# Optimization experiments

Measured on AMD Instinct MI355X. Metric: run time of the kernel, lower is better.

Reference implementation:

```python
import jax, jax.numpy as jnp
import numpy as np

EPS = 1e-6
TOP_K = 2


def setup_inputs() -> dict:
    key = jax.random.key(0)
    k0, k1, k2, k3, k4 = jax.random.split(key, 5)
    B, S, H, I, E = 1, 2048, 1024, 3584, 8
    return {
        "hidden_states": jax.random.normal(k0, (B, S, H), jnp.float32),
        "rms_weight": jnp.ones((H,), jnp.float32),
        "gate_w": jax.random.normal(k1, (E, H), jnp.float32) * (H ** -0.5),
        "w1": jax.random.normal(k2, (E, I, H), jnp.float32) * (H ** -0.5),
        "w2": jax.random.normal(k3, (E, H, I), jnp.float32) * (I ** -0.5),
        "w3": jax.random.normal(k4, (E, I, H), jnp.float32) * (H ** -0.5),
    }


def reference(hidden_states, rms_weight, gate_w, w1, w2, w3):
    B, S, H = hidden_states.shape
    E = gate_w.shape[0]
    # RMSNorm (fp32 internally, matches _RMSNorm)
    x = hidden_states.astype(jnp.float32)
    var = jnp.mean(x * x, axis=-1, keepdims=True)
    h = rms_weight * (x * jax.lax.rsqrt(var + EPS))  # [B,S,H]
    # Router: softmax over experts, top-k, renormalize
    logits = jnp.einsum('bsh,eh->bse', h, gate_w)
    scores = jax.nn.softmax(logits.astype(jnp.float32), axis=-1)
    top_w, top_i = jax.lax.top_k(scores, TOP_K)        # [B,S,K]
    top_w = top_w / jnp.sum(top_w, axis=-1, keepdims=True)
    top_w = top_w.astype(h.dtype)
    # Per-token combine weight for every expert: cw[t,e]
    hf = h.reshape(-1, H)                               # [T,H]
    oh = jax.nn.one_hot(top_i.reshape(-1, TOP_K), E, dtype=h.dtype)  # [T,K,E]
    cw = jnp.einsum('tke,tk->te', oh, top_w.reshape(-1, TOP_K))       # [T,E]
    # SwiGLU expert MLPs, batched over experts (dense dispatch; weights zero out unrouted tokens)
    a = jnp.einsum('th,eih->eti', hf, w1)               # [E,T,I]
    g = jnp.einsum('th,eih->eti', hf, w3)               # [E,T,I]
    eo = jnp.einsum('eti,ehi->eth', jax.nn.silu(a) * g, w2)  # [E,T,H]
    out = jnp.einsum('eth,te->th', eo, cw)              # [T,H]
    return hidden_states + out.reshape(B, S, H)
```

## Files before the change

### kernel.cpp

```cpp
#include <hip/hip_runtime.h>
#include <hip/hip_bf16.h>
#include <stdint.h>

#define T_TOK 2048
#define HDIM  1024
#define IDIM  3584
#define NEXP  8
#define NROWS 4096

typedef __attribute__((ext_vector_type(8))) short bf16x8;
typedef __attribute__((ext_vector_type(4))) float f32x4;
typedef __attribute__((ext_vector_type(4))) unsigned int u32x4;

__device__ __forceinline__ unsigned short f2bf(float f){
  union { float f; unsigned u; } v; v.f = f;
  unsigned r = v.u + 0x7FFFu + ((v.u >> 16) & 1u);
  return (unsigned short)(r >> 16);
}

__device__ __forceinline__ u32x4 pack8(float4 lo, float4 hi){
  union { unsigned short s[8]; u32x4 v; } u;
  u.s[0]=f2bf(lo.x); u.s[1]=f2bf(lo.y); u.s[2]=f2bf(lo.z); u.s[3]=f2bf(lo.w);
  u.s[4]=f2bf(hi.x); u.s[5]=f2bf(hi.y); u.s[6]=f2bf(hi.z); u.s[7]=f2bf(hi.w);
  return u.v;
}

__global__ __launch_bounds__(256) void k_rms_router(
    const float* __restrict__ x, const float* __restrict__ rmsw,
    const float* __restrict__ gw, unsigned short* __restrict__ h_bf,
    int* __restrict__ topk_i, float* __restrict__ topk_w, int* __restrict__ count)
{
  const int t = blockIdx.x, tid = threadIdx.x;
  const int lane = tid & 63, wid = tid >> 6;
  float4 x4 = reinterpret_cast<const float4*>(x)[t*256 + tid];
  float ss = x4.x*x4.x + x4.y*x4.y + x4.z*x4.z + x4.w*x4.w;
  #pragma unroll
  for (int o = 32; o >= 1; o >>= 1) ss += __shfl_xor(ss, o);
  __shared__ float sred[4];
  __shared__ float slog[32];
  if (lane == 0) sred[wid] = ss;
  __syncthreads();
  float inv = rsqrtf((sred[0]+sred[1]+sred[2]+sred[3]) * (1.0f/HDIM) + 1e-6f);
  float4 w4 = reinterpret_cast<const float4*>(rmsw)[tid];
  float h0 = x4.x*inv*w4.x, h1 = x4.y*inv*w4.y, h2 = x4.z*inv*w4.z, h3 = x4.w*inv*w4.w;
  ushort4 hb; hb.x = f2bf(h0); hb.y = f2bf(h1); hb.z = f2bf(h2); hb.w = f2bf(h3);
  reinterpret_cast<ushort4*>(h_bf)[t*256 + tid] = hb;
  #pragma unroll
  for (int e = 0; e < NEXP; e++){
    float4 g4 = reinterpret_cast<const float4*>(gw)[e*256 + tid];
    float v = h0*g4.x + h1*g4.y + h2*g4.z + h3*g4.w;
    #pragma unroll
    for (int o = 32; o >= 1; o >>= 1) v += __shfl_xor(v, o);
    if (lane == 0) slog[e*4 + wid] = v;
  }
  __syncthreads();
  if (tid == 0){
    float lg[NEXP];
    #pragma unroll
    for (int e = 0; e < NEXP; e++) lg[e] = slog[e*4]+slog[e*4+1]+slog[e*4+2]+slog[e*4+3];
    int i0 = 0;
    for (int e = 1; e < NEXP; e++) if (lg[e] > lg[i0]) i0 = e;
    int i1 = -1;
    for (int e = 0; e < NEXP; e++){ if (e == i0) continue; if (i1 < 0 || lg[e] > lg[i1]) i1 = e; }
    float m  = fmaxf(lg[i0], lg[i1]);
    float e0 = expf(lg[i0]-m), e1 = expf(lg[i1]-m);
    float s  = e0 + e1;
    topk_i[t*2] = i0; topk_i[t*2+1] = i1;
    topk_w[t*2] = e0/s; topk_w[t*2+1] = e1/s;
    atomicAdd(&count[i0], 1); atomicAdd(&count[i1], 1);
  }
}

__global__ void k_scan(const int* __restrict__ count, int* __restrict__ offset){
  if (threadIdx.x == 0){
    int o = 0;
    for (int e = 0; e < NEXP; e++){ offset[e] = o; o += count[e]; }
  }
}

__global__ __launch_bounds__(256) void k_scatter(
    const int* __restrict__ topk_i, const float* __restrict__ topk_w,
    const int* __restrict__ offset, int* __restrict__ cursor,
    int* __restrict__ token_of_row, float* __restrict__ wrow, int* __restrict__ slot_of)
{
  int t = blockIdx.x*256 + threadIdx.x;
  if (t >= T_TOK) return;
  #pragma unroll
  for (int k = 0; k < 2; k++){
    int e = topk_i[t*2+k];
    int pos = atomicAdd(&cursor[e], 1);
    int row = offset[e] + pos;
    token_of_row[row] = t;
    wrow[row] = topk_w[t*2+k];
    slot_of[t*2+k] = row;
  }
}

__global__ __launch_bounds__(256, 3) void k_mlp_in(
    const unsigned short* __restrict__ h_bf, const float* __restrict__ w1,
    const float* __restrict__ w3, const int* __restrict__ token_of_row,
    const int* __restrict__ count, const int* __restrict__ offset,
    unsigned short* __restrict__ act)
{
  int bx, by, bz;
  {
    int d = blockIdx.x + 16*(blockIdx.y + 56*blockIdx.z);
    int w = (d & 7)*896 + (d >> 3);
    bx = w & 15; int r = w >> 4; by = r % 56; bz = r / 56;
  }
  const int e = bz;
  const int tile = bx;
  const int cnt = count[e];
  if (tile * 128 >= cnt) return;
  const int off  = offset[e];
  const int row0 = off + tile*128;
  const int rend = off + cnt;
  const int col0 = by * 64;
  const int tid = threadIdx.x, lane = tid & 63, wid = tid >> 6;
  const int wave_r = wid >> 1, wave_c = wid & 1;

  __shared__ __align__(16) char sA [128*128];
  __shared__ __align__(16) char sB1[64*128];
  __shared__ __align__(16) char sB2[64*128];

  const int arow_base = tid >> 3;
  const int kseg = tid & 7;
  const unsigned short* aptr[4];
  #pragma unroll
  for (int j = 0; j < 4; j++){
    int r = row0 + arow_base + 32*j;
    aptr[j] = h_bf + (size_t)token_of_row[min(r, NROWS-1)]*HDIM + kseg*8;
  }
  const float* w1base = w1 + (size_t)e*IDIM*HDIM + (size_t)col0*HDIM + (size_t)arow_base*HDIM + kseg*8;
  const float* w3base = w3 + (size_t)e*IDIM*HDIM + (size_t)col0*HDIM + (size_t)arow_base*HDIM + kseg*8;

  u32x4  pa[4];
  float4 pb1[2][2], pb3[2][2];

  auto LOAD = [&](int kk){
    #pragma unroll
    for (int j = 0; j < 4; j++)
      pa[j] = *reinterpret_cast<const u32x4*>(aptr[j] + kk*64);
    #pragma unroll
    for (int j = 0; j < 2; j++){
      const float4* p1 = reinterpret_cast<const float4*>(w1base + (size_t)(32*j)*HDIM + kk*64);
      const float4* p3 = reinterpret_cast<const float4*>(w3base + (size_t)(32*j)*HDIM + kk*64);
      pb1[j][0] = p1[0]; pb1[j][1] = p1[1];
      pb3[j][0] = p3[0]; pb3[j][1] = p3[1];
    }
  };
  const int aswz = (kseg ^ (arow_base & 7)) << 4;
  auto STORE = [&](){
    #pragma unroll
    for (int j = 0; j < 4; j++)
      *reinterpret_cast<u32x4*>(sA + (arow_base + 32*j)*128 + aswz) = pa[j];
    #pragma unroll
    for (int j = 0; j < 2; j++){
      *reinterpret_cast<u32x4*>(sB1 + (arow_base + 32*j)*128 + aswz) = pack8(pb1[j][0], pb1[j][1]);
      *reinterpret_cast<u32x4*>(sB2 + (arow_base + 32*j)*128 + aswz) = pack8(pb3[j][0], pb3[j][1]);
    }
  };

  f32x4 acc_a[4][2], acc_g[4][2];
  #pragma unroll
  for (int m = 0; m < 4; m++)
    #pragma unroll
    for (int n = 0; n < 2; n++){
      acc_a[m][n] = (f32x4){0.f,0.f,0.f,0.f};
      acc_g[m][n] = (f32x4){0.f,0.f,0.f,0.f};
    }

  LOAD(0);
  for (int kk = 0; kk < HDIM/64; kk++){
    STORE();
    if (kk + 1 < HDIM/64) LOAD(kk+1);
    __syncthreads();
    #pragma unroll
    for (int ki = 0; ki < 2; ki++){
      bf16x8 af[4];
      #pragma unroll
      for (int m = 0; m < 4; m++){
        int row = wave_r*64 + m*16 + (lane&15);
        int slot = ki*4 + (lane>>4);
        af[m] = *reinterpret_cast<const bf16x8*>(sA + row*128 + ((slot ^ (row&7))<<4));
      }
      #pragma unroll
      for (int n = 0; n < 2; n++){
        int col = wave_c*32 + n*16 + (lane&15);
        int slot = ki*4 + (lane>>4);
        bf16x8 b1 = *reinterpret_cast<const bf16x8*>(sB1 + col*128 + ((slot ^ (col&7))<<4));
        bf16x8 b2 = *reinterpret_cast<const bf16x8*>(sB2 + col*128 + ((slot ^ (col&7))<<4));
        #pragma unroll
        for (int m = 0; m < 4; m++){
          acc_a[m][n] = __builtin_amdgcn_mfma_f32_16x16x32_bf16(af[m], b1, acc_a[m][n], 0,0,0);
          acc_g[m][n] = __builtin_amdgcn_mfma_f32_16x16x32_bf16(af[m], b2, acc_g[m][n], 0,0,0);
        }
      }
    }
    __syncthreads();
  }
  const int lcol = lane & 15, lrow4 = (lane >> 4) * 4;
  #pragma unroll
  for (int m = 0; m < 4; m++){
    #pragma unroll
    for (int n = 0; n < 2; n++){
      int gcol = col0 + wave_c*32 + n*16 + lcol;
      #pragma unroll
      for (int r = 0; r < 4; r++){
        int grow = row0 + wave_r*64 + m*16 + lrow4 + r;
        if (grow < rend){
          float a = acc_a[m][n][r], g = acc_g[m][n][r];
          float sig = 1.0f / (1.0f + __expf(-a));
          act[(size_t)grow*IDIM + gcol] = f2bf(a * sig * g);
        }
      }
    }
  }
}

__global__ __launch_bounds__(256, 4) void k_mlp_out(
    const unsigned short* __restrict__ act, const float* __restrict__ w2,
    const float* __restrict__ wrow, const int* __restrict__ count,
    const int* __restrict__ offset, float* __restrict__ eo)
{
  int bx, by, bz;
  {
    int d = blockIdx.x + 16*(blockIdx.y + 16*blockIdx.z);
    int w = (d & 7)*256 + (d >> 3);
    bx = w & 15; int r = w >> 4; by = r & 15; bz = r >> 4;
  }
  const int e = bz, tile = bx;
  const int cnt = count[e];
  if (tile*128 >= cnt) return;
  const int off = offset[e], row0 = off + tile*128, rend = off + cnt;
  const int col0 = by * 64;
  const int tid = threadIdx.x, lane = tid & 63, wid = tid >> 6;
  const int wave_r = wid >> 1, wave_c = wid & 1;

  __shared__ __align__(16) char sA[128*128];
  __shared__ __align__(16) char sB[64*128];

  const int arow_base = tid >> 3, kseg = tid & 7;
  const unsigned short* aptr[4];
  #pragma unroll
  for (int j = 0; j < 4; j++){
    int r = min(row0 + arow_base + 32*j, NROWS-1);
    aptr[j] = act + (size_t)r * IDIM + kseg*8;
  }
  const float* w2base = w2 + (size_t)e*HDIM*IDIM + (size_t)col0*IDIM + (size_t)arow_base*IDIM + kseg*8;

  u32x4  pa[4];
  float4 pb[2][2];

  auto LOAD = [&](int kk){
    #pragma unroll
    for (int j = 0; j < 4; j++)
      pa[j] = *reinterpret_cast<const u32x4*>(aptr[j] + kk*64);
    #pragma unroll
    for (int j = 0; j < 2; j++){
      const float4* p = reinterpret_cast<const float4*>(w2base + (size_t)(32*j)*IDIM + kk*64);
      pb[j][0] = p[0]; pb[j][1] = p[1];
    }
  };
  const int aswz = (kseg ^ (arow_base & 7)) << 4;
  auto STORE = [&](){
    #pragma unroll
    for (int j = 0; j < 4; j++)
      *reinterpret_cast<u32x4*>(sA + (arow_base + 32*j)*128 + aswz) = pa[j];
    #pragma unroll
    for (int j = 0; j < 2; j++)
      *reinterpret_cast<u32x4*>(sB + (arow_base + 32*j)*128 + aswz) = pack8(pb[j][0], pb[j][1]);
  };

  f32x4 acc[4][2];
  #pragma unroll
  for (int m = 0; m < 4; m++)
    #pragma unroll
    for (int n = 0; n < 2; n++) acc[m][n] = (f32x4){0.f,0.f,0.f,0.f};

  LOAD(0);
  for (int kk = 0; kk < IDIM/64; kk++){
    STORE();
    if (kk + 1 < IDIM/64) LOAD(kk+1);
    __syncthreads();
    #pragma unroll
    for (int ki = 0; ki < 2; ki++){
      bf16x8 af[4];
      #pragma unroll
      for (int m = 0; m < 4; m++){
        int row = wave_r*64 + m*16 + (lane&15);
        int slot = ki*4 + (lane>>4);
        af[m] = *reinterpret_cast<const bf16x8*>(sA + row*128 + ((slot ^ (row&7))<<4));
      }
      #pragma unroll
      for (int n = 0; n < 2; n++){
        int col = wave_c*32 + n*16 + (lane&15);
        int slot = ki*4 + (lane>>4);
        bf16x8 bf = *reinterpret_cast<const bf16x8*>(sB + col*128 + ((slot ^ (col&7))<<4));
        #pragma unroll
        for (int m = 0; m < 4; m++)
          acc[m][n] = __builtin_amdgcn_mfma_f32_16x16x32_bf16(af[m], bf, acc[m][n], 0,0,0);
      }
    }
    __syncthreads();
  }
  const int lcol = lane & 15, lrow4 = (lane >> 4) * 4;
  #pragma unroll
  for (int m = 0; m < 4; m++){
    #pragma unroll
    for (int n = 0; n < 2; n++){
      int gcol = col0 + wave_c*32 + n*16 + lcol;
      #pragma unroll
      for (int r = 0; r < 4; r++){
        int grow = row0 + wave_r*64 + m*16 + lrow4 + r;
        if (grow < rend){
          eo[(size_t)grow*HDIM + gcol] = acc[m][n][r] * wrow[grow];
        }
      }
    }
  }
}

__global__ __launch_bounds__(256) void k_combine(
    const float* __restrict__ x, const float* __restrict__ eo,
    const int* __restrict__ slot_of, float* __restrict__ out)
{
  const int t = blockIdx.x, tid = threadIdx.x;
  const int s0 = slot_of[t*2], s1 = slot_of[t*2+1];
  float4 xv = reinterpret_cast<const float4*>(x)[t*256 + tid];
  float4 a  = reinterpret_cast<const float4*>(eo)[s0*256 + tid];
  float4 b  = reinterpret_cast<const float4*>(eo)[s1*256 + tid];
  float4 ov;
  ov.x = xv.x + a.x + b.x;
  ov.y = xv.y + a.y + b.y;
  ov.z = xv.z + a.z + b.z;
  ov.w = xv.w + a.w + b.w;
  reinterpret_cast<float4*>(out)[t*256 + tid] = ov;
}

extern "C" void kernel_launch(void* const* d_in, const int* in_sizes, int n_in,
                              void* d_out, int out_size, void* d_ws, size_t ws_size,
                              hipStream_t stream)
{
  const float* x    = (const float*)d_in[0];
  const float* rmsw = (const float*)d_in[1];
  const float* gw   = (const float*)d_in[2];
  const float* w1   = (const float*)d_in[3];
  const float* w2   = (const float*)d_in[4];
  const float* w3   = (const float*)d_in[5];
  float* out = (float*)d_out;

  char* ws = (char*)d_ws;
  size_t o = 0;
  auto alloc = [&](size_t bytes) -> void* {
    void* p = ws + o;
    o += (bytes + 255) & ~(size_t)255;
    return p;
  };
  unsigned short* h_bf   = (unsigned short*)alloc((size_t)T_TOK*HDIM*2);
  int*   topk_i          = (int*)  alloc(T_TOK*2*4);
  float* topk_w          = (float*)alloc(T_TOK*2*4);
  int*   counters        = (int*)  alloc(64*4);
  int*   token_of_row    = (int*)  alloc(NROWS*4);
  float* wrow            = (float*)alloc(NROWS*4);
  int*   slot_of         = (int*)  alloc(T_TOK*2*4);
  unsigned short* act    = (unsigned short*)alloc((size_t)NROWS*IDIM*2);
  float* eo              = (float*)alloc((size_t)NROWS*HDIM*4);
  int* count  = counters;
  int* cursor = counters + 8;
  int* offset = counters + 16;

  hipMemsetAsync(counters, 0, 64*4, stream);
  k_rms_router<<<T_TOK, 256, 0, stream>>>(x, rmsw, gw, h_bf, topk_i, topk_w, count);
  k_scan<<<1, 64, 0, stream>>>(count, offset);
  k_scatter<<<(T_TOK+255)/256, 256, 0, stream>>>(topk_i, topk_w, offset, cursor,
                                                 token_of_row, wrow, slot_of);
  k_mlp_in <<<dim3(16, IDIM/64, NEXP), 256, 0, stream>>>(h_bf, w1, w3, token_of_row,
                                                         count, offset, act);
  k_mlp_out<<<dim3(16, HDIM/64, NEXP), 256, 0, stream>>>(act, w2, wrow, count, offset, eo);
  k_combine<<<T_TOK, 256, 0, stream>>>(x, eo, slot_of, out);
}
```

Baseline: 357.9 us.

## Deepen register prefetch to two stages in expert GEMMs and use packed bf16 conversion

Both expert MLP kernels now keep two k-steps of global loads in flight in registers (A/B sets) instead of one, so more global latency is hidden behind MFMA work. The float-to-bf16 packing now uses the paired __float22bfloat162_rn intrinsic in place of manual bit rounding. To make room for the extra prefetch registers, the occupancy hints in launch_bounds drop from 3 to 2 and from 4 to 3 blocks per CU. The cost is fewer resident waves and an extra barrier pair per iteration.

Result: slower. 384.8 us (+7.5%).

```diff
diff --git a/kernel.cpp b/kernel.cpp
--- a/kernel.cpp
+++ b/kernel.cpp
@@ -19,9 +19,11 @@
 }
 
 __device__ __forceinline__ u32x4 pack8(float4 lo, float4 hi){
-  union { unsigned short s[8]; u32x4 v; } u;
-  u.s[0]=f2bf(lo.x); u.s[1]=f2bf(lo.y); u.s[2]=f2bf(lo.z); u.s[3]=f2bf(lo.w);
-  u.s[4]=f2bf(hi.x); u.s[5]=f2bf(hi.y); u.s[6]=f2bf(hi.z); u.s[7]=f2bf(hi.w);
+  union { __hip_bfloat162 b2[4]; u32x4 v; } u;
+  u.b2[0] = __float22bfloat162_rn(float2{lo.x, lo.y});
+  u.b2[1] = __float22bfloat162_rn(float2{lo.z, lo.w});
+  u.b2[2] = __float22bfloat162_rn(float2{hi.x, hi.y});
+  u.b2[3] = __float22bfloat162_rn(float2{hi.z, hi.w});
   return u.v;
 }
 
@@ -96,7 +98,7 @@
   }
 }
 
-__global__ __launch_bounds__(256, 3) void k_mlp_in(
+__global__ __launch_bounds__(256, 2) void k_mlp_in(
     const unsigned short* __restrict__ h_bf, const float* __restrict__ w1,
     const float* __restrict__ w3, const int* __restrict__ token_of_row,
     const int* __restrict__ count, const int* __restrict__ offset,
@@ -134,32 +136,31 @@
   const float* w1base = w1 + (size_t)e*IDIM*HDIM + (size_t)col0*HDIM + (size_t)arow_base*HDIM + kseg*8;
   const float* w3base = w3 + (size_t)e*IDIM*HDIM + (size_t)col0*HDIM + (size_t)arow_base*HDIM + kseg*8;
 
-  u32x4  pa[4];
-  float4 pb1[2][2], pb3[2][2];
-
-  auto LOAD = [&](int kk){
-    #pragma unroll
-    for (int j = 0; j < 4; j++)
-      pa[j] = *reinterpret_cast<const u32x4*>(aptr[j] + kk*64);
-    #pragma unroll
-    for (int j = 0; j < 2; j++){
-      const float4* p1 = reinterpret_cast<const float4*>(w1base + (size_t)(32*j)*HDIM + kk*64);
-      const float4* p3 = reinterpret_cast<const float4*>(w3base + (size_t)(32*j)*HDIM + kk*64);
-      pb1[j][0] = p1[0]; pb1[j][1] = p1[1];
-      pb3[j][0] = p3[0]; pb3[j][1] = p3[1];
-    }
-  };
+  u32x4  paA[4], paB[4];
+  float4 pb1A[2][2], pb3A[2][2], pb1B[2][2], pb3B[2][2];
+
+  #define LOAD_SET(pa, pb1, pb3, kk)                                                 \
+    { _Pragma("unroll")                                                              \
+      for (int j = 0; j < 4; j++)                                                    \
+        pa[j] = *reinterpret_cast<const u32x4*>(aptr[j] + (kk)*64);                  \
+      _Pragma("unroll")                                                              \
+      for (int j = 0; j < 2; j++){                                                   \
+        const float4* p1 = reinterpret_cast<const float4*>(w1base + (size_t)(32*j)*HDIM + (kk)*64); \
+        const float4* p3 = reinterpret_cast<const float4*>(w3base + (size_t)(32*j)*HDIM + (kk)*64); \
+        pb1[j][0] = p1[0]; pb1[j][1] = p1[1];                                        \
+        pb3[j][0] = p3[0]; pb3[j][1] = p3[1];                                        \
+      } }
+
   const int aswz = (kseg ^ (arow_base & 7)) << 4;
-  auto STORE = [&](){
-    #pragma unroll
-    for (int j = 0; j < 4; j++)
-      *reinterpret_cast<u32x4*>(sA + (arow_base + 32*j)*128 + aswz) = pa[j];
-    #pragma unroll
-    for (int j = 0; j < 2; j++){
-      *reinterpret_cast<u32x4*>(sB1 + (arow_base + 32*j)*128 + aswz) = pack8(pb1[j][0], pb1[j][1]);
-      *reinterpret_cast<u32x4*>(sB2 + (arow_base + 32*j)*128 + aswz) = pack8(pb3[j][0], pb3[j][1]);
-    }
-  };
+  #define STORE_SET(pa, pb1, pb3)                                                    \
+    { _Pragma("unroll")                                                              \
+      for (int j = 0; j < 4; j++)                                                    \
+        *reinterpret_cast<u32x4*>(sA + (arow_base + 32*j)*128 + aswz) = pa[j];       \
+      _Pragma("unroll")                                                              \
+      for (int j = 0; j < 2; j++){                                                   \
+        *reinterpret_cast<u32x4*>(sB1 + (arow_base + 32*j)*128 + aswz) = pack8(pb1[j][0], pb1[j][1]); \
+        *reinterpret_cast<u32x4*>(sB2 + (arow_base + 32*j)*128 + aswz) = pack8(pb3[j][0], pb3[j][1]); \
+      } }
 
   f32x4 acc_a[4][2], acc_g[4][2];
   #pragma unroll
@@ -170,33 +171,42 @@
       acc_g[m][n] = (f32x4){0.f,0.f,0.f,0.f};
     }
 
-  LOAD(0);
-  for (int kk = 0; kk < HDIM/64; kk++){
-    STORE();
-    if (kk + 1 < HDIM/64) LOAD(kk+1);
-    __syncthreads();
-    #pragma unroll
-    for (int ki = 0; ki < 2; ki++){
-      bf16x8 af[4];
-      #pragma unroll
-      for (int m = 0; m < 4; m++){
-        int row = wave_r*64 + m*16 + (lane&15);
-        int slot = ki*4 + (lane>>4);
-        af[m] = *reinterpret_cast<const bf16x8*>(sA + row*128 + ((slot ^ (row&7))<<4));
-      }
-      #pragma unroll
-      for (int n = 0; n < 2; n++){
-        int col = wave_c*32 + n*16 + (lane&15);
-        int slot = ki*4 + (lane>>4);
-        bf16x8 b1 = *reinterpret_cast<const bf16x8*>(sB1 + col*128 + ((slot ^ (col&7))<<4));
-        bf16x8 b2 = *reinterpret_cast<const bf16x8*>(sB2 + col*128 + ((slot ^ (col&7))<<4));
-        #pragma unroll
-        for (int m = 0; m < 4; m++){
-          acc_a[m][n] = __builtin_amdgcn_mfma_f32_16x16x32_bf16(af[m], b1, acc_a[m][n], 0,0,0);
-          acc_g[m][n] = __builtin_amdgcn_mfma_f32_16x16x32_bf16(af[m], b2, acc_g[m][n], 0,0,0);
-        }
-      }
-    }
+  #define COMPUTE()                                                                  \
+    { _Pragma("unroll")                                                              \
+      for (int ki = 0; ki < 2; ki++){                                                \
+        bf16x8 af[4];                                                                \
+        _Pragma("unroll")                                                            \
+        for (int m = 0; m < 4; m++){                                                 \
+          int row = wave_r*64 + m*16 + (lane&15);                                    \
+          int slot = ki*4 + (lane>>4);                                               \
+          af[m] = *reinterpret_cast<const bf16x8*>(sA + row*128 + ((slot ^ (row&7))<<4)); \
+        }                                                                            \
+        _Pragma("unroll")                                                            \
+        for (int n = 0; n < 2; n++){                                                 \
+          int col = wave_c*32 + n*16 + (lane&15);                                    \
+          int slot = ki*4 + (lane>>4);                                               \
+          bf16x8 b1 = *reinterpret_cast<const bf16x8*>(sB1 + col*128 + ((slot ^ (col&7))<<4)); \
+          bf16x8 b2 = *reinterpret_cast<const bf16x8*>(sB2 + col*128 + ((slot ^ (col&7))<<4)); \
+          _Pragma("unroll")                                                          \
+          for (int m = 0; m < 4; m++){                                               \
+            acc_a[m][n] = __builtin_amdgcn_mfma_f32_16x16x32_bf16(af[m], b1, acc_a[m][n], 0,0,0); \
+            acc_g[m][n] = __builtin_amdgcn_mfma_f32_16x16x32_bf16(af[m], b2, acc_g[m][n], 0,0,0); \
+          }                                                                          \
+        }                                                                            \
+      } }
+
+  LOAD_SET(paA, pb1A, pb3A, 0);
+  LOAD_SET(paB, pb1B, pb3B, 1);
+  for (int kk = 0; kk < HDIM/64; kk += 2){
+    STORE_SET(paA, pb1A, pb3A);
+    __syncthreads();
+    if (kk + 2 < HDIM/64) LOAD_SET(paA, pb1A, pb3A, kk+2);
+    COMPUTE();
+    __syncthreads();
+    STORE_SET(paB, pb1B, pb3B);
+    __syncthreads();
+    if (kk + 3 < HDIM/64) LOAD_SET(paB, pb1B, pb3B, kk+3);
+    COMPUTE();
     __syncthreads();
   }
   const int lcol = lane & 15, lrow4 = (lane >> 4) * 4;
@@ -216,9 +226,12 @@
       }
     }
   }
-}
-
-__global__ __launch_bounds__(256, 4) void k_mlp_out(
+  #undef LOAD_SET
+  #undef STORE_SET
+  #undef COMPUTE
+}
+
+__global__ __launch_bounds__(256, 3) void k_mlp_out(
     const unsigned short* __restrict__ act, const float* __restrict__ w2,
     const float* __restrict__ wrow, const int* __restrict__ count,
     const int* __restrict__ offset, float* __restrict__ eo)
@@ -249,28 +262,27 @@
   }
   const float* w2base = w2 + (size_t)e*HDIM*IDIM + (size_t)col0*IDIM + (size_t)arow_base*IDIM + kseg*8;
 
-  u32x4  pa[4];
-  float4 pb[2][2];
-
-  auto LOAD = [&](int kk){
-    #pragma unroll
-    for (int j = 0; j < 4; j++)
-      pa[j] = *reinterpret_cast<const u32x4*>(aptr[j] + kk*64);
-    #pragma unroll
-    for (int j = 0; j < 2; j++){
-      const float4* p = reinterpret_cast<const float4*>(w2base + (size_t)(32*j)*IDIM + kk*64);
-      pb[j][0] = p[0]; pb[j][1] = p[1];
-    }
-  };
+  u32x4  paA[4], paB[4];
+  float4 pbA[2][2], pbB[2][2];
+
+  #define LOAD_SET(pa, pb, kk)                                                       \
+    { _Pragma("unroll")                                                              \
+      for (int j = 0; j < 4; j++)                                                    \
+        pa[j] = *reinterpret_cast<const u32x4*>(aptr[j] + (kk)*64);                  \
+      _Pragma("unroll")                                                              \
+      for (int j = 0; j < 2; j++){                                                   \
+        const float4* p = reinterpret_cast<const float4*>(w2base + (size_t)(32*j)*IDIM + (kk)*64); \
+        pb[j][0] = p[0]; pb[j][1] = p[1];                                            \
+      } }
+
   const int aswz = (kseg ^ (arow_base & 7)) << 4;
-  auto STORE = [&](){
-    #pragma unroll
-    for (int j = 0; j < 4; j++)
-      *reinterpret_cast<u32x4*>(sA + (arow_base + 32*j)*128 + aswz) = pa[j];
-    #pragma unroll
-    for (int j = 0; j < 2; j++)
-      *reinterpret_cast<u32x4*>(sB + (arow_base + 32*j)*128 + aswz) = pack8(pb[j][0], pb[j][1]);
-  };
+  #define STORE_SET(pa, pb)                                                          \
+    { _Pragma("unroll")                                                              \
+      for (int j = 0; j < 4; j++)                                                    \
+        *reinterpret_cast<u32x4*>(sA + (arow_base + 32*j)*128 + aswz) = pa[j];       \
+      _Pragma("unroll")                                                              \
+      for (int j = 0; j < 2; j++)                                                    \
+        *reinterpret_cast<u32x4*>(sB + (arow_base + 32*j)*128 + aswz) = pack8(pb[j][0], pb[j][1]); }
 
   f32x4 acc[4][2];
   #pragma unroll
@@ -278,30 +290,39 @@
     #pragma unroll
     for (int n = 0; n < 2; n++) acc[m][n] = (f32x4){0.f,0.f,0.f,0.f};
 
-  LOAD(0);
-  for (int kk = 0; kk < IDIM/64; kk++){
-    STORE();
-    if (kk + 1 < IDIM/64) LOAD(kk+1);
-    __syncthreads();
-    #pragma unroll
-    for (int ki = 0; ki < 2; ki++){
-      bf16x8 af[4];
-      #pragma unroll
-      for (int m = 0; m < 4; m++){
-        int row = wave_r*64 + m*16 + (lane&15);
-        int slot = ki*4 + (lane>>4);
-        af[m] = *reinterpret_cast<const bf16x8*>(sA + row*128 + ((slot ^ (row&7))<<4));
-      }
-      #pragma unroll
-      for (int n = 0; n < 2; n++){
-        int col = wave_c*32 + n*16 + (lane&15);
-        int slot = ki*4 + (lane>>4);
-        bf16x8 bf = *reinterpret_cast<const bf16x8*>(sB + col*128 + ((slot ^ (col&7))<<4));
-        #pragma unroll
-        for (int m = 0; m < 4; m++)
-          acc[m][n] = __builtin_amdgcn_mfma_f32_16x16x32_bf16(af[m], bf, acc[m][n], 0,0,0);
-      }
-    }
+  #define COMPUTE()                                                                  \
+    { _Pragma("unroll")                                                              \
+      for (int ki = 0; ki < 2; ki++){                                                \
+        bf16x8 af[4];                                                                \
+        _Pragma("unroll")                                                            \
+        for (int m = 0; m < 4; m++){                                                 \
+          int row = wave_r*64 + m*16 + (lane&15);                                    \
+          int slot = ki*4 + (lane>>4);                                               \
+          af[m] = *reinterpret_cast<const bf16x8*>(sA + row*128 + ((slot ^ (row&7))<<4)); \
+        }                                                                            \
+        _Pragma("unroll")                                                            \
+        for (int n = 0; n < 2; n++){                                                 \
+          int col = wave_c*32 + n*16 + (lane&15);                                    \
+          int slot = ki*4 + (lane>>4);                                               \
+          bf16x8 bf = *reinterpret_cast<const bf16x8*>(sB + col*128 + ((slot ^ (col&7))<<4)); \
+          _Pragma("unroll")                                                          \
+          for (int m = 0; m < 4; m++)                                                \
+            acc[m][n] = __builtin_amdgcn_mfma_f32_16x16x32_bf16(af[m], bf, acc[m][n], 0,0,0); \
+        }                                                                            \
+      } }
+
+  LOAD_SET(paA, pbA, 0);
+  LOAD_SET(paB, pbB, 1);
+  for (int kk = 0; kk < IDIM/64; kk += 2){
+    STORE_SET(paA, pbA);
+    __syncthreads();
+    if (kk + 2 < IDIM/64) LOAD_SET(paA, pbA, kk+2);
+    COMPUTE();
+    __syncthreads();
+    STORE_SET(paB, pbB);
+    __syncthreads();
+    if (kk + 3 < IDIM/64) LOAD_SET(paB, pbB, kk+3);
+    COMPUTE();
     __syncthreads();
   }
   const int lcol = lane & 15, lrow4 = (lane >> 4) * 4;
@@ -319,6 +340,9 @@
       }
     }
   }
+  #undef LOAD_SET
+  #undef STORE_SET
+  #undef COMPUTE
 }
 
 __global__ __launch_bounds__(256) void k_combine(
```

## Pre-convert expert weights to bf16 and stream tiles via global_load_lds

Applied to the files above, without the earlier changes.

When the workspace is large enough, w1/w3/w2 are first converted to bf16 into scratch buffers by a grid-stride conversion kernel. New GEMM kernels then load A and B tiles straight into LDS with global_load_lds, skipping the register round trip and the per-tile pack. They also use a 1D grid with expert-interleaved block ordering. This adds a full read plus half-size write of every weight each call, and the new GEMM loop has no register prefetch, so load latency is only hidden by occupancy. If the workspace is too small, the code falls back to the original fp32-weight kernels.

New measurement: 348.6 us. 2.6% less time.

```diff
diff --git a/kernel.cpp b/kernel.cpp
--- a/kernel.cpp
+++ b/kernel.cpp
@@ -7,21 +7,32 @@
 #define IDIM  3584
 #define NEXP  8
 #define NROWS 4096
+#define WELEM 29360128
 
 typedef __attribute__((ext_vector_type(8))) short bf16x8;
 typedef __attribute__((ext_vector_type(4))) float f32x4;
 typedef __attribute__((ext_vector_type(4))) unsigned int u32x4;
+
+typedef __attribute__((address_space(3))) unsigned lds_u32;
+typedef const __attribute__((address_space(1))) unsigned glb_u32;
+
+#define MFMA16 __builtin_amdgcn_mfma_f32_16x16x32_bf16
 
 __device__ __forceinline__ unsigned short f2bf(float f){
   union { float f; unsigned u; } v; v.f = f;
   unsigned r = v.u + 0x7FFFu + ((v.u >> 16) & 1u);
   return (unsigned short)(r >> 16);
 }
-
-__device__ __forceinline__ u32x4 pack8(float4 lo, float4 hi){
-  union { unsigned short s[8]; u32x4 v; } u;
-  u.s[0]=f2bf(lo.x); u.s[1]=f2bf(lo.y); u.s[2]=f2bf(lo.z); u.s[3]=f2bf(lo.w);
-  u.s[4]=f2bf(hi.x); u.s[5]=f2bf(hi.y); u.s[6]=f2bf(hi.z); u.s[7]=f2bf(hi.w);
+__device__ __forceinline__ unsigned cvt2(float a, float b){
+  __hip_bfloat162 h = __float22bfloat162_rn(float2{a, b});
+  return *reinterpret_cast<unsigned*>(&h);
+}
+__device__ __forceinline__ bf16x8 pack8(float4 lo, float4 hi){
+  union { __hip_bfloat162 b2[4]; bf16x8 v; } u;
+  u.b2[0] = __float22bfloat162_rn(float2{lo.x, lo.y});
+  u.b2[1] = __float22bfloat162_rn(float2{lo.z, lo.w});
+  u.b2[2] = __float22bfloat162_rn(float2{hi.x, hi.y});
+  u.b2[3] = __float22bfloat162_rn(float2{hi.z, hi.w});
   return u.v;
 }
 
@@ -96,7 +107,222 @@
   }
 }
 
-__global__ __launch_bounds__(256, 3) void k_mlp_in(
+__global__ __launch_bounds__(256) void k_cvt(
+    const float4* __restrict__ src, uint2* __restrict__ dst, int n4)
+{
+  int stride = gridDim.x * blockDim.x;
+  for (int i = blockIdx.x*blockDim.x + threadIdx.x; i < n4; i += stride){
+    float4 v = src[i];
+    dst[i] = make_uint2(cvt2(v.x, v.y), cvt2(v.z, v.w));
+  }
+}
+
+__global__ __launch_bounds__(256, 3) void k_mlp_in_bf(
+    const unsigned short* __restrict__ h_bf, const unsigned short* __restrict__ w1bf,
+    const unsigned short* __restrict__ w3bf, const int* __restrict__ token_of_row,
+    const int* __restrict__ count, const int* __restrict__ offset,
+    unsigned short* __restrict__ act)
+{
+  const int d = blockIdx.x;
+  const int e = d & 7;
+  const int q = d >> 3;
+  const int panel = q >> 4;
+  const int rt = q & 15;
+  const int cnt = count[e];
+  if (rt * 128 >= cnt) return;
+  const int off = offset[e], row0 = off + rt*128, rend = off + cnt;
+  const int col0 = panel * 64;
+  const int tid = threadIdx.x, lane = tid & 63, wid = tid >> 6;
+  const int wave_r = wid >> 1, wave_c = wid & 1;
+
+  __shared__ __align__(16) char sA [128*128];
+  __shared__ __align__(16) char sB1[64*128];
+  __shared__ __align__(16) char sB2[64*128];
+
+  const int srow = tid >> 3;
+  const int sg   = (tid & 7) ^ (srow & 7);
+
+  const unsigned short* aptr[4];
+  #pragma unroll
+  for (int j = 0; j < 4; j++){
+    int tok = token_of_row[min(row0 + srow + 32*j, NROWS-1)];
+    aptr[j] = h_bf + (size_t)tok*HDIM + sg*8;
+  }
+  const unsigned short* b1ptr[2];
+  const unsigned short* b3ptr[2];
+  #pragma unroll
+  for (int j = 0; j < 2; j++){
+    int col = col0 + srow + 32*j;
+    b1ptr[j] = w1bf + (size_t)(e*IDIM + col)*HDIM + sg*8;
+    b3ptr[j] = w3bf + (size_t)(e*IDIM + col)*HDIM + sg*8;
+  }
+
+  #define ISSUE(kk) {                                                                \
+    _Pragma("unroll")                                                                \
+    for (int j = 0; j < 4; j++)                                                      \
+      __builtin_amdgcn_global_load_lds((glb_u32*)(const void*)(aptr[j] + (kk)*64),   \
+          (lds_u32*)(void*)(sA + j*4096 + tid*16), 16, 0, 0);                        \
+    _Pragma("unroll")                                                                \
+    for (int j = 0; j < 2; j++){                                                     \
+      __builtin_amdgcn_global_load_lds((glb_u32*)(const void*)(b1ptr[j] + (kk)*64),  \
+          (lds_u32*)(void*)(sB1 + j*4096 + tid*16), 16, 0, 0);                       \
+      __builtin_amdgcn_global_load_lds((glb_u32*)(const void*)(b3ptr[j] + (kk)*64),  \
+          (lds_u32*)(void*)(sB2 + j*4096 + tid*16), 16, 0, 0);                       \
+    } }
+
+  f32x4 acc1[4][2], acc3[4][2];
+  #pragma unroll
+  for (int m = 0; m < 4; m++)
+    #pragma unroll
+    for (int n = 0; n < 2; n++){
+      acc1[m][n] = (f32x4){0.f,0.f,0.f,0.f};
+      acc3[m][n] = (f32x4){0.f,0.f,0.f,0.f};
+    }
+
+  for (int kk = 0; kk < HDIM/64; kk++){
+    ISSUE(kk);
+    __syncthreads();
+    #pragma unroll
+    for (int ki = 0; ki < 2; ki++){
+      bf16x8 af[4];
+      #pragma unroll
+      for (int m = 0; m < 4; m++){
+        int row = wave_r*64 + m*16 + (lane & 15);
+        int slot = ki*4 + (lane >> 4);
+        af[m] = *reinterpret_cast<const bf16x8*>(sA + row*128 + ((slot ^ (row&7))<<4));
+      }
+      #pragma unroll
+      for (int n = 0; n < 2; n++){
+        int col = wave_c*32 + n*16 + (lane & 15);
+        int slot = ki*4 + (lane >> 4);
+        bf16x8 b1 = *reinterpret_cast<const bf16x8*>(sB1 + col*128 + ((slot ^ (col&7))<<4));
+        bf16x8 b2 = *reinterpret_cast<const bf16x8*>(sB2 + col*128 + ((slot ^ (col&7))<<4));
+        #pragma unroll
+        for (int m = 0; m < 4; m++){
+          acc1[m][n] = MFMA16(af[m], b1, acc1[m][n], 0,0,0);
+          acc3[m][n] = MFMA16(af[m], b2, acc3[m][n], 0,0,0);
+        }
+      }
+    }
+    __syncthreads();
+  }
+
+  const int lcol = lane & 15, lrow4 = (lane >> 4) * 4;
+  #pragma unroll
+  for (int m = 0; m < 4; m++){
+    #pragma unroll
+    for (int n = 0; n < 2; n++){
+      int gcol = col0 + wave_c*32 + n*16 + lcol;
+      #pragma unroll
+      for (int r = 0; r < 4; r++){
+        int grow = row0 + wave_r*64 + m*16 + lrow4 + r;
+        if (grow < rend){
+          float a = acc1[m][n][r], g = acc3[m][n][r];
+          float sig = 1.0f / (1.0f + __expf(-a));
+          act[(size_t)grow*IDIM + gcol] = f2bf(a * sig * g);
+        }
+      }
+    }
+  }
+  #undef ISSUE
+}
+
+__global__ __launch_bounds__(256, 4) void k_mlp_out_bf(
+    const unsigned short* __restrict__ act, const unsigned short* __restrict__ w2bf,
+    const float* __restrict__ wrow, const int* __restrict__ count,
+    const int* __restrict__ offset, float* __restrict__ eo)
+{
+  const int d = blockIdx.x;
+  const int e = d & 7;
+  const int q = d >> 3;
+  const int panel = q >> 4;
+  const int rt = q & 15;
+  const int cnt = count[e];
+  if (rt * 128 >= cnt) return;
+  const int off = offset[e], row0 = off + rt*128, rend = off + cnt;
+  const int col0 = panel * 64;
+  const int tid = threadIdx.x, lane = tid & 63, wid = tid >> 6;
+  const int wave_r = wid >> 1, wave_c = wid & 1;
+
+  __shared__ __align__(16) char sA[128*128];
+  __shared__ __align__(16) char sB[64*128];
+
+  const int srow = tid >> 3;
+  const int sg   = (tid & 7) ^ (srow & 7);
+
+  const unsigned short* aptr[4];
+  #pragma unroll
+  for (int j = 0; j < 4; j++){
+    int r = min(row0 + srow + 32*j, NROWS-1);
+    aptr[j] = act + (size_t)r*IDIM + sg*8;
+  }
+  const unsigned short* bptr[2];
+  #pragma unroll
+  for (int j = 0; j < 2; j++){
+    int col = col0 + srow + 32*j;
+    bptr[j] = w2bf + (size_t)(e*HDIM + col)*IDIM + sg*8;
+  }
+
+  #define ISSUE(kk) {                                                                \
+    _Pragma("unroll")                                                                \
+    for (int j = 0; j < 4; j++)                                                      \
+      __builtin_amdgcn_global_load_lds((glb_u32*)(const void*)(aptr[j] + (kk)*64),   \
+          (lds_u32*)(void*)(sA + j*4096 + tid*16), 16, 0, 0);                        \
+    _Pragma("unroll")                                                                \
+    for (int j = 0; j < 2; j++)                                                      \
+      __builtin_amdgcn_global_load_lds((glb_u32*)(const void*)(bptr[j] + (kk)*64),   \
+          (lds_u32*)(void*)(sB + j*4096 + tid*16), 16, 0, 0); }
+
+  f32x4 acc[4][2];
+  #pragma unroll
+  for (int m = 0; m < 4; m++)
+    #pragma unroll
+    for (int n = 0; n < 2; n++) acc[m][n] = (f32x4){0.f,0.f,0.f,0.f};
+
+  for (int kk = 0; kk < IDIM/64; kk++){
+    ISSUE(kk);
+    __syncthreads();
+    #pragma unroll
+    for (int ki = 0; ki < 2; ki++){
+      bf16x8 af[4];
+      #pragma unroll
+      for (int m = 0; m < 4; m++){
+        int row = wave_r*64 + m*16 + (lane & 15);
+        int slot = ki*4 + (lane >> 4);
+        af[m] = *reinterpret_cast<const bf16x8*>(sA + row*128 + ((slot ^ (row&7))<<4));
+      }
+      #pragma unroll
+      for (int n = 0; n < 2; n++){
+        int col = wave_c*32 + n*16 + (lane & 15);
+        int slot = ki*4 + (lane >> 4);
+        bf16x8 fb = *reinterpret_cast<const bf16x8*>(sB + col*128 + ((slot ^ (col&7))<<4));
+        #pragma unroll
+        for (int m = 0; m < 4; m++)
+          acc[m][n] = MFMA16(af[m], fb, acc[m][n], 0,0,0);
+      }
+    }
+    __syncthreads();
+  }
+
+  const int lcol = lane & 15, lrow4 = (lane >> 4) * 4;
+  #pragma unroll
+  for (int m = 0; m < 4; m++){
+    #pragma unroll
+    for (int n = 0; n < 2; n++){
+      int gcol = col0 + wave_c*32 + n*16 + lcol;
+      #pragma unroll
+      for (int r = 0; r < 4; r++){
+        int grow = row0 + wave_r*64 + m*16 + lrow4 + r;
+        if (grow < rend){
+          eo[(size_t)grow*HDIM + gcol] = acc[m][n][r] * wrow[grow];
+        }
+      }
+    }
+  }
+  #undef ISSUE
+}
+
+__global__ __launch_bounds__(256, 2) void k_mlp_in_fb(
     const unsigned short* __restrict__ h_bf, const float* __restrict__ w1,
     const float* __restrict__ w3, const int* __restrict__ token_of_row,
     const int* __restrict__ count, const int* __restrict__ offset,
@@ -108,8 +334,7 @@
     int w = (d & 7)*896 + (d >> 3);
     bx = w & 15; int r = w >> 4; by = r % 56; bz = r / 56;
   }
-  const int e = bz;
-  const int tile = bx;
+  const int e = bz, tile = bx;
   const int cnt = count[e];
   if (tile * 128 >= cnt) return;
   const int off  = offset[e];
@@ -156,8 +381,8 @@
       *reinterpret_cast<u32x4*>(sA + (arow_base + 32*j)*128 + aswz) = pa[j];
     #pragma unroll
     for (int j = 0; j < 2; j++){
-      *reinterpret_cast<u32x4*>(sB1 + (arow_base + 32*j)*128 + aswz) = pack8(pb1[j][0], pb1[j][1]);
-      *reinterpret_cast<u32x4*>(sB2 + (arow_base + 32*j)*128 + aswz) = pack8(pb3[j][0], pb3[j][1]);
+      *reinterpret_cast<bf16x8*>(sB1 + (arow_base + 32*j)*128 + aswz) = pack8(pb1[j][0], pb1[j][1]);
+      *reinterpret_cast<bf16x8*>(sB2 + (arow_base + 32*j)*128 + aswz) = pack8(pb3[j][0], pb3[j][1]);
     }
   };
 
@@ -192,8 +417,8 @@
         bf16x8 b2 = *reinterpret_cast<const bf16x8*>(sB2 + col*128 + ((slot ^ (col&7))<<4));
         #pragma unroll
         for (int m = 0; m < 4; m++){
-          acc_a[m][n] = __builtin_amdgcn_mfma_f32_16x16x32_bf16(af[m], b1, acc_a[m][n], 0,0,0);
-          acc_g[m][n] = __builtin_amdgcn_mfma_f32_16x16x32_bf16(af[m], b2, acc_g[m][n], 0,0,0);
+          acc_a[m][n] = MFMA16(af[m], b1, acc_a[m][n], 0,0,0);
+          acc_g[m][n] = MFMA16(af[m], b2, acc_g[m][n], 0,0,0);
         }
       }
     }
@@ -218,7 +443,7 @@
   }
 }
 
-__global__ __launch_bounds__(256, 4) void k_mlp_out(
+__global__ __launch_bounds__(256, 3) void k_mlp_out_fb(
     const unsigned short* __restrict__ act, const float* __restrict__ w2,
     const float* __restrict__ wrow, const int* __restrict__ count,
     const int* __restrict__ offset, float* __restrict__ eo)
@@ -269,7 +494,7 @@
       *reinterpret_cast<u32x4*>(sA + (arow_base + 32*j)*128 + aswz) = pa[j];
     #pragma unroll
     for (int j = 0; j < 2; j++)
-      *reinterpret_cast<u32x4*>(sB + (arow_base + 32*j)*128 + aswz) = pack8(pb[j][0], pb[j][1]);
+      *reinterpret_cast<bf16x8*>(sB + (arow_base + 32*j)*128 + aswz) = pack8(pb[j][0], pb[j][1]);
   };
 
   f32x4 acc[4][2];
@@ -296,10 +521,10 @@
       for (int n = 0; n < 2; n++){
         int col = wave_c*32 + n*16 + (lane&15);
         int slot = ki*4 + (lane>>4);
-        bf16x8 bf = *reinterpret_cast<const bf16x8*>(sB + col*128 + ((slot ^ (col&7))<<4));
+        bf16x8 fb = *reinterpret_cast<const bf16x8*>(sB + col*128 + ((slot ^ (col&7))<<4));
         #pragma unroll
         for (int m = 0; m < 4; m++)
-          acc[m][n] = __builtin_amdgcn_mfma_f32_16x16x32_bf16(af[m], bf, acc[m][n], 0,0,0);
+          acc[m][n] = MFMA16(af[m], fb, acc[m][n], 0,0,0);
       }
     }
     __syncthreads();
@@ -370,13 +595,28 @@
   int* cursor = counters + 8;
   int* offset = counters + 16;
 
+  const size_t wbf_bytes = (size_t)2 * WELEM * 2;
+  bool bfpath = (ws_size >= o + wbf_bytes);
+  unsigned short* w1bfp = (unsigned short*)(ws + o);
+  unsigned short* w3bfp = w1bfp + WELEM;
+  unsigned short* w2bfp = w1bfp;
+
   hipMemsetAsync(counters, 0, 64*4, stream);
   k_rms_router<<<T_TOK, 256, 0, stream>>>(x, rmsw, gw, h_bf, topk_i, topk_w, count);
   k_scan<<<1, 64, 0, stream>>>(count, offset);
   k_scatter<<<(T_TOK+255)/256, 256, 0, stream>>>(topk_i, topk_w, offset, cursor,
                                                  token_of_row, wrow, slot_of);
-  k_mlp_in <<<dim3(16, IDIM/64, NEXP), 256, 0, stream>>>(h_bf, w1, w3, token_of_row,
-                                                         count, offset, act);
-  k_mlp_out<<<dim3(16, HDIM/64, NEXP), 256, 0, stream>>>(act, w2, wrow, count, offset, eo);
+  if (bfpath){
+    k_cvt<<<2048, 256, 0, stream>>>((const float4*)w1, (uint2*)w1bfp, WELEM/4);
+    k_cvt<<<2048, 256, 0, stream>>>((const float4*)w3, (uint2*)w3bfp, WELEM/4);
+    k_mlp_in_bf<<<7168, 256, 0, stream>>>(h_bf, w1bfp, w3bfp, token_of_row,
+                                          count, offset, act);
+    k_cvt<<<2048, 256, 0, stream>>>((const float4*)w2, (uint2*)w2bfp, WELEM/4);
+    k_mlp_out_bf<<<2048, 256, 0, stream>>>(act, w2bfp, wrow, count, offset, eo);
+  } else {
+    k_mlp_in_fb <<<dim3(16, 56, 8), 256, 0, stream>>>(h_bf, w1, w3, token_of_row,
+                                                      count, offset, act);
+    k_mlp_out_fb<<<dim3(16, 16, 8), 256, 0, stream>>>(act, w2, wrow, count, offset, eo);
+  }
   k_combine<<<T_TOK, 256, 0, stream>>>(x, eo, slot_of, out);
 }
```
